# Performance work log

Measured on AMD Instinct MI355X. Metric: run time of the kernel, lower is better.

The kernel has to match this reference:

```python
import jax, jax.numpy as jnp
import numpy as np
import math

B, S, D = 4, 2048, 768
H = 12
DH = D // H  # 64
NEG = -1e10

def setup_inputs() -> dict:
    key = jax.random.key(0)
    ks = jax.random.split(key, 8)
    scale = 0.02
    return {
        "hidden_states": jax.random.normal(ks[0], (B, S, D), dtype=jnp.float32),
        "attention_mask": jnp.zeros((B, 1, 1, S), dtype=jnp.float32),
        "Wq": jax.random.normal(ks[1], (D, D), dtype=jnp.float32) * scale,
        "bq": jnp.zeros((D,), dtype=jnp.float32),
        "Wk": jax.random.normal(ks[2], (D, D), dtype=jnp.float32) * scale,
        "bk": jnp.zeros((D,), dtype=jnp.float32),
        "Wv": jax.random.normal(ks[3], (D, D), dtype=jnp.float32) * scale,
        "bv": jnp.zeros((D,), dtype=jnp.float32),
    }

def reference(hidden_states, attention_mask, Wq, bq, Wk, bk, Wv, bv):
    # Linear projections; note attention_mask is accepted but unused, matching the torch module.
    def split_heads(x):  # [B,S,D] -> [B,H,S,DH]
        return x.reshape(B, S, H, DH).transpose(0, 2, 1, 3)
    q = split_heads(hidden_states @ Wq + bq)
    k = split_heads(hidden_states @ Wk + bk)
    v = split_heads(hidden_states @ Wv + bv)
    scores = jnp.einsum("bhqd,bhkd->bhqk", q, k) / math.sqrt(DH)
    causal = jnp.tril(jnp.ones((S, S), dtype=bool))  # masked_fill(mask==0, -1e10)
    scores = jnp.where(causal, scores, NEG)
    probs = jax.nn.softmax(scores, axis=-1)
    # dropout prob = 0.0 (eval) -> identity
    ctx = jnp.einsum("bhqk,bhkd->bhqd", probs, v)
    return ctx.transpose(0, 2, 1, 3).reshape(B, S, D)
```

## Files before the change

kernel.cpp:

```cpp
#include <hip/hip_runtime.h>
#include <hip/hip_bf16.h>

#define B_  4
#define S_  2048
#define D_  768
#define H_  12
#define DH_ 64

typedef __bf16 bf16;
typedef __attribute__((ext_vector_type(8))) __bf16 bf16x8;
typedef __attribute__((ext_vector_type(4))) __bf16 bf16x4;
typedef __attribute__((ext_vector_type(4))) float floatx4;

__global__ __launch_bounds__(256) void cvt_f32_bf16(const float* __restrict__ in,
                                                    bf16* __restrict__ out, int n4) {
    int i = blockIdx.x * 256 + threadIdx.x;
    if (i < n4) {
        float4 v = ((const float4*)in)[i];
        bf16x4 o;
        o[0] = (bf16)v.x; o[1] = (bf16)v.y; o[2] = (bf16)v.z; o[3] = (bf16)v.w;
        *(bf16x4*)(out + (size_t)i * 4) = o;
    }
}

__global__ __launch_bounds__(256) void w_transpose(const float* __restrict__ w0,
                                                   const float* __restrict__ w1,
                                                   const float* __restrict__ w2,
                                                   bf16* __restrict__ Wt)
{
    const int which = blockIdx.z;
    const float* W = (which == 0) ? w0 : (which == 1 ? w1 : w2);
    bf16* dst = Wt + (size_t)which * D_ * D_;
    __shared__ bf16 t[64 * 72];
    const int k0 = blockIdx.x * 64, n0 = blockIdx.y * 64;
    const int tid = threadIdx.x;
    {
        int r = tid >> 2;
        int c0 = (tid & 3) * 16;
        #pragma unroll
        for (int q = 0; q < 4; q++) {
            float4 v = *(const float4*)(W + (size_t)(k0 + r) * D_ + n0 + c0 + q * 4);
            t[(c0 + q * 4 + 0) * 72 + r] = (bf16)v.x;
            t[(c0 + q * 4 + 1) * 72 + r] = (bf16)v.y;
            t[(c0 + q * 4 + 2) * 72 + r] = (bf16)v.z;
            t[(c0 + q * 4 + 3) * 72 + r] = (bf16)v.w;
        }
    }
    __syncthreads();
    {
        int n = tid >> 3, seg = tid & 7;
        *(bf16x8*)(dst + (size_t)(n0 + n) * D_ + k0 + seg * 8) =
            *(const bf16x8*)(t + n * 72 + seg * 8);
        *(bf16x8*)(dst + (size_t)(n0 + n + 32) * D_ + k0 + seg * 8) =
            *(const bf16x8*)(t + (n + 32) * 72 + seg * 8);
    }
}

__global__ __launch_bounds__(256) void qkv_gemm(
    const bf16* __restrict__ Xb, const bf16* __restrict__ Wt,
    const float* __restrict__ bq, const float* __restrict__ bk,
    const float* __restrict__ bv, bf16* __restrict__ QKV)
{
    const int which = blockIdx.z;
    const bf16* Wm = Wt + (size_t)which * D_ * D_;
    const float* bias = (which == 0) ? bq : (which == 1 ? bk : bv);
    bf16* out = QKV + (size_t)which * B_ * H_ * S_ * DH_;

    __shared__ bf16 As[128 * 72];
    __shared__ bf16 Bs[64 * 72];

    const int tid  = threadIdx.x;
    const int wave = tid >> 6, lane = tid & 63;
    const int wr = wave >> 1, wc = wave & 1;
    const int g = lane >> 4, ln = lane & 15;
    const int m0 = blockIdx.x * 128, n0 = blockIdx.y * 64;

    int arow[4], aseg[4], brow[2], bseg[2];
    #pragma unroll
    for (int t = 0; t < 4; t++) { int c = tid + t * 256; arow[t] = c >> 3; aseg[t] = c & 7; }
    #pragma unroll
    for (int t = 0; t < 2; t++) { int c = tid + t * 256; brow[t] = c >> 3; bseg[t] = c & 7; }

    floatx4 acc[4][2];
    #pragma unroll
    for (int i = 0; i < 4; i++)
        #pragma unroll
        for (int j = 0; j < 2; j++)
            acc[i][j] = (floatx4){0.f, 0.f, 0.f, 0.f};

    bf16x8 apf[4], bpf[2];
    #pragma unroll
    for (int t = 0; t < 4; t++)
        apf[t] = *(const bf16x8*)(Xb + (size_t)(m0 + arow[t]) * D_ + aseg[t] * 8);
    #pragma unroll
    for (int t = 0; t < 2; t++)
        bpf[t] = *(const bf16x8*)(Wm + (size_t)(n0 + brow[t]) * D_ + bseg[t] * 8);

    for (int k0 = 0; k0 < D_; k0 += 64) {
        __syncthreads();
        #pragma unroll
        for (int t = 0; t < 4; t++)
            *(bf16x8*)(As + arow[t] * 72 + aseg[t] * 8) = apf[t];
        #pragma unroll
        for (int t = 0; t < 2; t++)
            *(bf16x8*)(Bs + brow[t] * 72 + bseg[t] * 8) = bpf[t];
        __syncthreads();
        if (k0 + 64 < D_) {
            #pragma unroll
            for (int t = 0; t < 4; t++)
                apf[t] = *(const bf16x8*)(Xb + (size_t)(m0 + arow[t]) * D_ + k0 + 64 + aseg[t] * 8);
            #pragma unroll
            for (int t = 0; t < 2; t++)
                bpf[t] = *(const bf16x8*)(Wm + (size_t)(n0 + brow[t]) * D_ + k0 + 64 + bseg[t] * 8);
        }
        #pragma unroll
        for (int ks = 0; ks < 2; ks++) {
            bf16x8 af[4], bfr[2];
            #pragma unroll
            for (int i = 0; i < 4; i++)
                af[i] = *(const bf16x8*)(As + (wr * 64 + i * 16 + ln) * 72 + ks * 32 + g * 8);
            #pragma unroll
            for (int j = 0; j < 2; j++)
                bfr[j] = *(const bf16x8*)(Bs + (wc * 32 + j * 16 + ln) * 72 + ks * 32 + g * 8);
            #pragma unroll
            for (int i = 0; i < 4; i++)
                #pragma unroll
                for (int j = 0; j < 2; j++)
                    acc[i][j] = __builtin_amdgcn_mfma_f32_16x16x32_bf16(af[i], bfr[j], acc[i][j], 0, 0, 0);
        }
    }

    const int h = blockIdx.y;
    #pragma unroll
    for (int i = 0; i < 4; i++) {
        #pragma unroll
        for (int j = 0; j < 2; j++) {
            int col = n0 + wc * 32 + j * 16 + ln;
            float bv_ = bias[col];
            int dh = col & 63;
            int rowbase = m0 + wr * 64 + i * 16 + g * 4;
            int b = rowbase >> 11, s0 = rowbase & 2047;
            if (which == 2) {
                bf16x4 o;
                #pragma unroll
                for (int r = 0; r < 4; r++) o[r] = (bf16)(acc[i][j][r] + bv_);
                *(bf16x4*)(out + ((size_t)((b * H_ + h) * DH_ + dh)) * S_ + s0) = o;
            } else {
                #pragma unroll
                for (int r = 0; r < 4; r++)
                    out[(((size_t)(b * H_ + h) * S_ + s0 + r) << 6) + dh] =
                        (bf16)(acc[i][j][r] + bv_);
            }
        }
    }
}

__global__ __launch_bounds__(256) void attn_kernel(const bf16* __restrict__ QKV,
                                                   float* __restrict__ out)
{
    const int qt = 31 - blockIdx.x;
    const int bh = blockIdx.y;
    const int b = bh / H_, h = bh % H_;
    const size_t MAT = (size_t)B_ * H_ * S_ * DH_;
    const bf16* Q  = QKV +           (size_t)bh * S_ * DH_;
    const bf16* K  = QKV + MAT +     (size_t)bh * S_ * DH_;
    const bf16* Vt = QKV + 2 * MAT + (size_t)bh * S_ * DH_;

    __shared__ bf16 Ks[64 * 72];
    __shared__ bf16 Vts[64 * 72];
    __shared__ bf16 Ps[4][16 * 72];

    const int tid  = threadIdx.x;
    const int wave = tid >> 6, lane = tid & 63;
    const int g = lane >> 4, ln = lane & 15;
    const int srow = tid >> 3, sseg = tid & 7;

    bf16x8 qf[2];
    {
        const bf16* qrow = Q + (size_t)(qt * 64 + wave * 16 + ln) * DH_;
        qf[0] = *(const bf16x8*)(qrow + g * 8);
        qf[1] = *(const bf16x8*)(qrow + 32 + g * 8);
    }

    bf16x8 ones;
    #pragma unroll
    for (int i = 0; i < 8; i++) ones[i] = (bf16)1.0f;

    floatx4 accO[4];
    #pragma unroll
    for (int j = 0; j < 4; j++) accO[j] = (floatx4){0.f, 0.f, 0.f, 0.f};
    floatx4 accL = (floatx4){0.f, 0.f, 0.f, 0.f};

    const bf16* kp0 = K  + (size_t)srow * DH_ + sseg * 8;
    const bf16* kp1 = kp0 + 32 * DH_;
    const bf16* vp0 = Vt + (size_t)srow * S_ + sseg * 8;
    const bf16* vp1 = vp0 + (size_t)32 * S_;

    bf16x8 ka = *(const bf16x8*)kp0;
    bf16x8 kb = *(const bf16x8*)kp1;
    bf16x8 va = *(const bf16x8*)vp0;
    bf16x8 vb = *(const bf16x8*)vp1;

    for (int kt = 0; kt <= qt; ++kt) {
        __syncthreads();
        *(bf16x8*)(Ks  + srow * 72 + sseg * 8) = ka;
        *(bf16x8*)(Ks  + (srow + 32) * 72 + sseg * 8) = kb;
        *(bf16x8*)(Vts + srow * 72 + sseg * 8) = va;
        *(bf16x8*)(Vts + (srow + 32) * 72 + sseg * 8) = vb;
        __syncthreads();
        if (kt < qt) {
            ka = *(const bf16x8*)(kp0 + (size_t)(kt + 1) * 64 * DH_);
            kb = *(const bf16x8*)(kp1 + (size_t)(kt + 1) * 64 * DH_);
            va = *(const bf16x8*)(vp0 + (kt + 1) * 64);
            vb = *(const bf16x8*)(vp1 + (kt + 1) * 64);
        }

        floatx4 accS[4];
        #pragma unroll
        for (int j = 0; j < 4; j++) accS[j] = (floatx4){0.f, 0.f, 0.f, 0.f};
        #pragma unroll
        for (int j = 0; j < 4; j++) {
            #pragma unroll
            for (int c = 0; c < 2; c++) {
                bf16x8 kf = *(const bf16x8*)(Ks + (j * 16 + ln) * 72 + c * 32 + g * 8);
                accS[j] = __builtin_amdgcn_mfma_f32_16x16x32_bf16(qf[c], kf, accS[j], 0, 0, 0);
            }
        }

        #pragma unroll
        for (int j = 0; j < 4; j++)
            #pragma unroll
            for (int r = 0; r < 4; r++)
                accS[j][r] = __expf(accS[j][r] * 0.125f);
        if (kt == qt) {
            #pragma unroll
            for (int j = 0; j < 4; j++) {
                int krow = j * 16 + ln;
                #pragma unroll
                for (int r = 0; r < 4; r++) {
                    int qrow = wave * 16 + g * 4 + r;
                    if (krow > qrow) accS[j][r] = 0.f;
                }
            }
        }

        bf16* Pw = Ps[wave];
        #pragma unroll
        for (int j = 0; j < 4; j++)
            #pragma unroll
            for (int r = 0; r < 4; r++)
                Pw[(g * 4 + r) * 72 + j * 16 + ln] = (bf16)accS[j][r];

        #pragma unroll
        for (int c = 0; c < 2; c++) {
            bf16x8 pf = *(const bf16x8*)(Pw + ln * 72 + c * 32 + g * 8);
            accL = __builtin_amdgcn_mfma_f32_16x16x32_bf16(pf, ones, accL, 0, 0, 0);
            #pragma unroll
            for (int j = 0; j < 4; j++) {
                bf16x8 vf = *(const bf16x8*)(Vts + (j * 16 + ln) * 72 + c * 32 + g * 8);
                accO[j] = __builtin_amdgcn_mfma_f32_16x16x32_bf16(pf, vf, accO[j], 0, 0, 0);
            }
        }
    }

    float inv[4];
    #pragma unroll
    for (int r = 0; r < 4; r++) inv[r] = 1.0f / accL[r];
    #pragma unroll
    for (int j = 0; j < 4; j++) {
        int dh = j * 16 + ln;
        #pragma unroll
        for (int r = 0; r < 4; r++) {
            int q = qt * 64 + wave * 16 + g * 4 + r;
            out[((size_t)(b * S_ + q)) * D_ + h * DH_ + dh] = accO[j][r] * inv[r];
        }
    }
}

extern "C" void kernel_launch(void* const* d_in, const int* in_sizes, int n_in,
                              void* d_out, int out_size, void* d_ws, size_t ws_size,
                              hipStream_t stream) {
    const float* hs = (const float*)d_in[0];
    const float* Wq = (const float*)d_in[2];
    const float* bq = (const float*)d_in[3];
    const float* Wk = (const float*)d_in[4];
    const float* bk = (const float*)d_in[5];
    const float* Wv = (const float*)d_in[6];
    const float* bv = (const float*)d_in[7];
    float* out = (float*)d_out;

    bf16* Xb  = (bf16*)d_ws;
    bf16* Wt  = Xb + (size_t)8192 * 768;
    bf16* QKV = Wt + (size_t)3 * 768 * 768;

    cvt_f32_bf16<<<6144, 256, 0, stream>>>(hs, Xb, 1572864);
    w_transpose<<<dim3(12, 12, 3), 256, 0, stream>>>(Wq, Wk, Wv, Wt);
    qkv_gemm<<<dim3(64, 12, 3), 256, 0, stream>>>(Xb, Wt, bq, bk, bv, QKV);
    attn_kernel<<<dim3(32, 48), 256, 0, stream>>>(QKV, out);
}
```

Baseline: 227.3 us.

## Split causal attention KV range into chunks with a reduction pass; widen QKV GEMM tile

The attention kernel now splits each query tile's key range into chunks of up to 8 key tiles, giving 80 blocks per head instead of 32 with a more even work size. Multi-chunk tiles write bf16 partial outputs and row sums to workspace, and a new reduce kernel adds them and normalizes. The QKV GEMM tile grows from 128x64 to 128x128 to reuse each A load across more columns. The cost is an extra launch, extra global traffic for the partials, bf16 rounding of the partial sums, and more accumulator registers in the GEMM.

```diff
diff --git a/kernel.cpp b/kernel.cpp
--- a/kernel.cpp
+++ b/kernel.cpp
@@ -11,6 +11,13 @@
 typedef __attribute__((ext_vector_type(8))) __bf16 bf16x8;
 typedef __attribute__((ext_vector_type(4))) __bf16 bf16x4;
 typedef __attribute__((ext_vector_type(4))) float floatx4;
+
+__device__ __forceinline__ int chunk_off(int qt) {
+    if (qt < 8)  return qt;
+    if (qt < 16) return 8 + 2 * (qt - 8);
+    if (qt < 24) return 24 + 3 * (qt - 16);
+    return 48 + 4 * (qt - 24);
+}
 
 __global__ __launch_bounds__(256) void cvt_f32_bf16(const float* __restrict__ in,
                                                     bf16* __restrict__ out, int n4) {
@@ -67,77 +74,71 @@
     bf16* out = QKV + (size_t)which * B_ * H_ * S_ * DH_;
 
     __shared__ bf16 As[128 * 72];
-    __shared__ bf16 Bs[64 * 72];
+    __shared__ bf16 Bs[128 * 72];
 
     const int tid  = threadIdx.x;
     const int wave = tid >> 6, lane = tid & 63;
     const int wr = wave >> 1, wc = wave & 1;
     const int g = lane >> 4, ln = lane & 15;
-    const int m0 = blockIdx.x * 128, n0 = blockIdx.y * 64;
-
-    int arow[4], aseg[4], brow[2], bseg[2];
-    #pragma unroll
-    for (int t = 0; t < 4; t++) { int c = tid + t * 256; arow[t] = c >> 3; aseg[t] = c & 7; }
-    #pragma unroll
-    for (int t = 0; t < 2; t++) { int c = tid + t * 256; brow[t] = c >> 3; bseg[t] = c & 7; }
-
-    floatx4 acc[4][2];
+    const int m0 = blockIdx.x * 128, n0 = blockIdx.y * 128;
+
+    floatx4 acc[4][4];
     #pragma unroll
     for (int i = 0; i < 4; i++)
         #pragma unroll
-        for (int j = 0; j < 2; j++)
+        for (int j = 0; j < 4; j++)
             acc[i][j] = (floatx4){0.f, 0.f, 0.f, 0.f};
 
-    bf16x8 apf[4], bpf[2];
-    #pragma unroll
-    for (int t = 0; t < 4; t++)
-        apf[t] = *(const bf16x8*)(Xb + (size_t)(m0 + arow[t]) * D_ + aseg[t] * 8);
-    #pragma unroll
-    for (int t = 0; t < 2; t++)
-        bpf[t] = *(const bf16x8*)(Wm + (size_t)(n0 + brow[t]) * D_ + bseg[t] * 8);
+    int row_[4], seg_[4];
+    #pragma unroll
+    for (int t = 0; t < 4; t++) { int fc = tid + t * 256; row_[t] = fc >> 3; seg_[t] = fc & 7; }
+
+    bf16x8 apf[4], bpf[4];
+    #pragma unroll
+    for (int t = 0; t < 4; t++) {
+        apf[t] = *(const bf16x8*)(Xb + (size_t)(m0 + row_[t]) * D_ + seg_[t] * 8);
+        bpf[t] = *(const bf16x8*)(Wm + (size_t)(n0 + row_[t]) * D_ + seg_[t] * 8);
+    }
 
     for (int k0 = 0; k0 < D_; k0 += 64) {
         __syncthreads();
         #pragma unroll
-        for (int t = 0; t < 4; t++)
-            *(bf16x8*)(As + arow[t] * 72 + aseg[t] * 8) = apf[t];
-        #pragma unroll
-        for (int t = 0; t < 2; t++)
-            *(bf16x8*)(Bs + brow[t] * 72 + bseg[t] * 8) = bpf[t];
+        for (int t = 0; t < 4; t++) {
+            *(bf16x8*)(As + row_[t] * 72 + seg_[t] * 8) = apf[t];
+            *(bf16x8*)(Bs + row_[t] * 72 + seg_[t] * 8) = bpf[t];
+        }
         __syncthreads();
         if (k0 + 64 < D_) {
             #pragma unroll
-            for (int t = 0; t < 4; t++)
-                apf[t] = *(const bf16x8*)(Xb + (size_t)(m0 + arow[t]) * D_ + k0 + 64 + aseg[t] * 8);
-            #pragma unroll
-            for (int t = 0; t < 2; t++)
-                bpf[t] = *(const bf16x8*)(Wm + (size_t)(n0 + brow[t]) * D_ + k0 + 64 + bseg[t] * 8);
+            for (int t = 0; t < 4; t++) {
+                apf[t] = *(const bf16x8*)(Xb + (size_t)(m0 + row_[t]) * D_ + k0 + 64 + seg_[t] * 8);
+                bpf[t] = *(const bf16x8*)(Wm + (size_t)(n0 + row_[t]) * D_ + k0 + 64 + seg_[t] * 8);
+            }
         }
         #pragma unroll
         for (int ks = 0; ks < 2; ks++) {
-            bf16x8 af[4], bfr[2];
+            bf16x8 af[4], bfr[4];
             #pragma unroll
             for (int i = 0; i < 4; i++)
                 af[i] = *(const bf16x8*)(As + (wr * 64 + i * 16 + ln) * 72 + ks * 32 + g * 8);
             #pragma unroll
-            for (int j = 0; j < 2; j++)
-                bfr[j] = *(const bf16x8*)(Bs + (wc * 32 + j * 16 + ln) * 72 + ks * 32 + g * 8);
+            for (int j = 0; j < 4; j++)
+                bfr[j] = *(const bf16x8*)(Bs + (wc * 64 + j * 16 + ln) * 72 + ks * 32 + g * 8);
             #pragma unroll
             for (int i = 0; i < 4; i++)
                 #pragma unroll
-                for (int j = 0; j < 2; j++)
+                for (int j = 0; j < 4; j++)
                     acc[i][j] = __builtin_amdgcn_mfma_f32_16x16x32_bf16(af[i], bfr[j], acc[i][j], 0, 0, 0);
         }
     }
 
-    const int h = blockIdx.y;
     #pragma unroll
     for (int i = 0; i < 4; i++) {
         #pragma unroll
-        for (int j = 0; j < 2; j++) {
-            int col = n0 + wc * 32 + j * 16 + ln;
+        for (int j = 0; j < 4; j++) {
+            int col = n0 + wc * 64 + j * 16 + ln;
             float bv_ = bias[col];
-            int dh = col & 63;
+            int h = col >> 6, dh = col & 63;
             int rowbase = m0 + wr * 64 + i * 16 + g * 4;
             int b = rowbase >> 11, s0 = rowbase & 2047;
             if (which == 2) {
@@ -155,12 +156,24 @@
     }
 }
 
-__global__ __launch_bounds__(256) void attn_kernel(const bf16* __restrict__ QKV,
-                                                   float* __restrict__ out)
+__global__ __launch_bounds__(256) void attn_chunk(const bf16* __restrict__ QKV,
+                                                  float* __restrict__ out,
+                                                  bf16* __restrict__ Opart,
+                                                  float* __restrict__ Lpart)
 {
-    const int qt = 31 - blockIdx.x;
+    const int cid = 79 - blockIdx.x;
     const int bh = blockIdx.y;
     const int b = bh / H_, h = bh % H_;
+
+    int qt, c;
+    if (cid < 8)       { qt = cid; c = 0; }
+    else if (cid < 24) { qt = 8 + ((cid - 8) >> 1); c = (cid - 8) & 1; }
+    else if (cid < 48) { int t3 = cid - 24; qt = 16 + t3 / 3; c = t3 - (qt - 16) * 3; }
+    else               { int t4 = cid - 48; qt = 24 + (t4 >> 2); c = t4 & 3; }
+    const int nch = (qt >> 3) + 1;
+    const int kt0 = c * 8;
+    const int kt1 = min(kt0 + 7, qt);
+
     const size_t MAT = (size_t)B_ * H_ * S_ * DH_;
     const bf16* Q  = QKV +           (size_t)bh * S_ * DH_;
     const bf16* K  = QKV + MAT +     (size_t)bh * S_ * DH_;
@@ -191,28 +204,28 @@
     for (int j = 0; j < 4; j++) accO[j] = (floatx4){0.f, 0.f, 0.f, 0.f};
     floatx4 accL = (floatx4){0.f, 0.f, 0.f, 0.f};
 
-    const bf16* kp0 = K  + (size_t)srow * DH_ + sseg * 8;
-    const bf16* kp1 = kp0 + 32 * DH_;
-    const bf16* vp0 = Vt + (size_t)srow * S_ + sseg * 8;
-    const bf16* vp1 = vp0 + (size_t)32 * S_;
-
-    bf16x8 ka = *(const bf16x8*)kp0;
-    bf16x8 kb = *(const bf16x8*)kp1;
-    bf16x8 va = *(const bf16x8*)vp0;
-    bf16x8 vb = *(const bf16x8*)vp1;
-
-    for (int kt = 0; kt <= qt; ++kt) {
+    const bf16* kptr = K  + (size_t)(kt0 * 64 + srow) * DH_ + sseg * 8;
+    const bf16* vptr = Vt + (size_t)srow * S_ + kt0 * 64 + sseg * 8;
+
+    bf16x8 ka = *(const bf16x8*)kptr;
+    bf16x8 kb = *(const bf16x8*)(kptr + 32 * DH_);
+    bf16x8 va = *(const bf16x8*)vptr;
+    bf16x8 vb = *(const bf16x8*)(vptr + (size_t)32 * S_);
+
+    for (int kt = kt0; kt <= kt1; ++kt) {
         __syncthreads();
         *(bf16x8*)(Ks  + srow * 72 + sseg * 8) = ka;
         *(bf16x8*)(Ks  + (srow + 32) * 72 + sseg * 8) = kb;
         *(bf16x8*)(Vts + srow * 72 + sseg * 8) = va;
         *(bf16x8*)(Vts + (srow + 32) * 72 + sseg * 8) = vb;
         __syncthreads();
-        if (kt < qt) {
-            ka = *(const bf16x8*)(kp0 + (size_t)(kt + 1) * 64 * DH_);
-            kb = *(const bf16x8*)(kp1 + (size_t)(kt + 1) * 64 * DH_);
-            va = *(const bf16x8*)(vp0 + (kt + 1) * 64);
-            vb = *(const bf16x8*)(vp1 + (kt + 1) * 64);
+        if (kt < kt1) {
+            kptr += 64 * DH_;
+            vptr += 64;
+            ka = *(const bf16x8*)kptr;
+            kb = *(const bf16x8*)(kptr + 32 * DH_);
+            va = *(const bf16x8*)vptr;
+            vb = *(const bf16x8*)(vptr + (size_t)32 * S_);
         }
 
         floatx4 accS[4];
@@ -221,9 +234,9 @@
         #pragma unroll
         for (int j = 0; j < 4; j++) {
             #pragma unroll
-            for (int c = 0; c < 2; c++) {
-                bf16x8 kf = *(const bf16x8*)(Ks + (j * 16 + ln) * 72 + c * 32 + g * 8);
-                accS[j] = __builtin_amdgcn_mfma_f32_16x16x32_bf16(qf[c], kf, accS[j], 0, 0, 0);
+            for (int cc = 0; cc < 2; cc++) {
+                bf16x8 kf = *(const bf16x8*)(Ks + (j * 16 + ln) * 72 + cc * 32 + g * 8);
+                accS[j] = __builtin_amdgcn_mfma_f32_16x16x32_bf16(qf[cc], kf, accS[j], 0, 0, 0);
             }
         }
 
@@ -252,27 +265,88 @@
                 Pw[(g * 4 + r) * 72 + j * 16 + ln] = (bf16)accS[j][r];
 
         #pragma unroll
-        for (int c = 0; c < 2; c++) {
-            bf16x8 pf = *(const bf16x8*)(Pw + ln * 72 + c * 32 + g * 8);
+        for (int cc = 0; cc < 2; cc++) {
+            bf16x8 pf = *(const bf16x8*)(Pw + ln * 72 + cc * 32 + g * 8);
             accL = __builtin_amdgcn_mfma_f32_16x16x32_bf16(pf, ones, accL, 0, 0, 0);
             #pragma unroll
             for (int j = 0; j < 4; j++) {
-                bf16x8 vf = *(const bf16x8*)(Vts + (j * 16 + ln) * 72 + c * 32 + g * 8);
+                bf16x8 vf = *(const bf16x8*)(Vts + (j * 16 + ln) * 72 + cc * 32 + g * 8);
                 accO[j] = __builtin_amdgcn_mfma_f32_16x16x32_bf16(pf, vf, accO[j], 0, 0, 0);
             }
         }
     }
 
+    if (nch == 1) {
+        float inv[4];
+        #pragma unroll
+        for (int r = 0; r < 4; r++) inv[r] = 1.0f / accL[r];
+        #pragma unroll
+        for (int j = 0; j < 4; j++) {
+            int dh = j * 16 + ln;
+            #pragma unroll
+            for (int r = 0; r < 4; r++) {
+                int q = qt * 64 + wave * 16 + g * 4 + r;
+                out[((size_t)(b * S_ + q)) * D_ + h * DH_ + dh] = accO[j][r] * inv[r];
+            }
+        }
+    } else {
+        const int chunk = bh * 80 + chunk_off(qt) + c;
+        bf16x8 p0, p1;
+        #pragma unroll
+        for (int e = 0; e < 8; e++) {
+            p0[e] = (bf16)accO[e >> 2][e & 3];
+            p1[e] = (bf16)accO[2 + (e >> 2)][e & 3];
+        }
+        bf16* dst = Opart + (size_t)chunk * 4096 + tid * 16;
+        *(bf16x8*)dst = p0;
+        *(bf16x8*)(dst + 8) = p1;
+        if (ln == 0) {
+            #pragma unroll
+            for (int r = 0; r < 4; r++)
+                Lpart[chunk * 64 + wave * 16 + g * 4 + r] = accL[r];
+        }
+    }
+}
+
+__global__ __launch_bounds__(256) void attn_reduce(const bf16* __restrict__ Opart,
+                                                   const float* __restrict__ Lpart,
+                                                   float* __restrict__ out)
+{
+    const int qt = 8 + blockIdx.x;
+    const int bh = blockIdx.y;
+    const int b = bh / H_, h = bh % H_;
+    const int nch = (qt >> 3) + 1;
+    const int cb = bh * 80 + chunk_off(qt);
+
+    const int tid  = threadIdx.x;
+    const int wave = tid >> 6, lane = tid & 63;
+    const int g = lane >> 4, ln = lane & 15;
+
+    float o[16];
+    #pragma unroll
+    for (int e = 0; e < 16; e++) o[e] = 0.f;
+    float ls[4] = {0.f, 0.f, 0.f, 0.f};
+
+    for (int cidx = 0; cidx < nch; cidx++) {
+        const bf16* p = Opart + (size_t)(cb + cidx) * 4096 + tid * 16;
+        bf16x8 v0 = *(const bf16x8*)p;
+        bf16x8 v1 = *(const bf16x8*)(p + 8);
+        #pragma unroll
+        for (int e = 0; e < 8; e++) { o[e] += (float)v0[e]; o[8 + e] += (float)v1[e]; }
+        #pragma unroll
+        for (int r = 0; r < 4; r++)
+            ls[r] += Lpart[(cb + cidx) * 64 + wave * 16 + g * 4 + r];
+    }
     float inv[4];
     #pragma unroll
-    for (int r = 0; r < 4; r++) inv[r] = 1.0f / accL[r];
+    for (int r = 0; r < 4; r++) inv[r] = 1.0f / ls[r];
     #pragma unroll
     for (int j = 0; j < 4; j++) {
         int dh = j * 16 + ln;
         #pragma unroll
         for (int r = 0; r < 4; r++) {
             int q = qt * 64 + wave * 16 + g * 4 + r;
-            out[((size_t)(b * S_ + q)) * D_ + h * DH_ + dh] = accO[j][r] * inv[r];
+            out[((size_t)(b * S_ + q)) * D_ + h * DH_ + dh] = o[j * 4 + r] * inv[r];
         }
     }
 }
@@ -289,12 +363,15 @@
     const float* bv = (const float*)d_in[7];
     float* out = (float*)d_out;
 
-    bf16* Xb  = (bf16*)d_ws;
-    bf16* Wt  = Xb + (size_t)8192 * 768;
-    bf16* QKV = Wt + (size_t)3 * 768 * 768;
+    bf16* Xb    = (bf16*)d_ws;
+    bf16* Wt    = Xb + (size_t)8192 * 768;
+    bf16* QKV   = Wt + (size_t)3 * 768 * 768;
+    bf16* Opart = QKV + (size_t)3 * B_ * H_ * S_ * DH_;
+    float* Lpart = (float*)(Opart + (size_t)3840 * 4096);
 
     cvt_f32_bf16<<<6144, 256, 0, stream>>>(hs, Xb, 1572864);
     w_transpose<<<dim3(12, 12, 3), 256, 0, stream>>>(Wq, Wk, Wv, Wt);
-    qkv_gemm<<<dim3(64, 12, 3), 256, 0, stream>>>(Xb, Wt, bq, bk, bv, QKV);
-    attn_kernel<<<dim3(32, 48), 256, 0, stream>>>(QKV, out);
-}
+    qkv_gemm<<<dim3(64, 6, 3), 256, 0, stream>>>(Xb, Wt, bq, bk, bv, QKV);
+    attn_chunk<<<dim3(80, 48), 256, 0, stream>>>(QKV, out, Opart, Lpart);
+    attn_reduce<<<dim3(24, 48), 256, 0, stream>>>(Opart, Lpart, out);
+}
```

After: 202.1 us. 1.12x faster.
